# Optimization experiments

Measured on AMD Instinct MI355X. Metric: run time of the kernel, lower is better.

The kernel has to match this reference:

```python
import jax, jax.numpy as jnp
import numpy as np

N_NODES = 100000


def _gcn_conv(x, W, b, src, dst, deg_inv_sqrt):
    # linear transform first (PyG GCNConv order): [N, F] @ [F, H]
    h = x @ W
    # symmetric normalization per edge: deg^-1/2[src] * deg^-1/2[dst]
    norm = deg_inv_sqrt[src] * deg_inv_sqrt[dst]
    msg = h[src] * norm[:, None]  # [E, H]
    out = jax.ops.segment_sum(msg, dst, num_segments=N_NODES)
    return out + b


def setup_inputs() -> dict:
    key = jax.random.key(0)
    k1, k2, k3, k4 = jax.random.split(key, 4)
    F_IN, H = 512, 512
    E = 800000
    x = jax.random.normal(k1, (N_NODES, F_IN), dtype=jnp.float32)
    edge_index = jax.random.randint(k2, (2, E), 0, N_NODES, dtype=jnp.int64)
    W1 = jax.random.normal(k3, (F_IN, H), dtype=jnp.float32) * (1.0 / np.sqrt(F_IN))
    b1 = jnp.zeros((H,), dtype=jnp.float32)
    W2 = jax.random.normal(k4, (H, H), dtype=jnp.float32) * (1.0 / np.sqrt(H))
    b2 = jnp.zeros((H,), dtype=jnp.float32)
    return {"x": x, "edge_index": edge_index, "W1": W1, "b1": b1, "W2": W2, "b2": b2}


def reference(x, edge_index, W1, b1, W2, b2):
    # add self loops (PyG GCNConv default add_self_loops=True)
    loop = jnp.arange(N_NODES, dtype=edge_index.dtype)
    src = jnp.concatenate([edge_index[0], loop])
    dst = jnp.concatenate([edge_index[1], loop])
    # degree of destination nodes (including self loops)
    deg = jax.ops.segment_sum(jnp.ones_like(dst, dtype=x.dtype), dst, num_segments=N_NODES)
    deg_inv_sqrt = jnp.where(deg > 0, jax.lax.rsqrt(jnp.maximum(deg, 1.0)), 0.0)
    h = jax.nn.relu(_gcn_conv(x, W1, b1, src, dst, deg_inv_sqrt))
    # dropout is identity at inference (training=False)
    out = _gcn_conv(h, W2, b2, src, dst, deg_inv_sqrt)
    return out
```

## Files before the change

### kernel.cpp

```cpp
#include <hip/hip_runtime.h>

#define N_NODES 100000
#define E_EDGES 800000
#define E_TOT   900000
#define F 512

typedef __attribute__((ext_vector_type(8))) short short8;
typedef __attribute__((ext_vector_type(4))) float f32x4;
typedef unsigned int u32;

__device__ __forceinline__ float bfu(unsigned int u) {
    union { unsigned int i; float f; } c; c.i = u << 16; return c.f;
}
__device__ __forceinline__ unsigned short f2b(float f) {
    union { float f; unsigned int u; } c; c.f = f;
    return (unsigned short)((c.u + 0x7fffu + ((c.u >> 16) & 1u)) >> 16);
}
__device__ __forceinline__ float fbits(unsigned int u) {
    union { unsigned int i; float f; } c; c.i = u; return c.f;
}
__device__ __forceinline__ unsigned int bits(float f) {
    union { float f; unsigned int i; } c; c.f = f; return c.i;
}
__device__ __forceinline__ void gload_lds16(const void* g, void* l) {
    __builtin_amdgcn_global_load_lds(
        (const __attribute__((address_space(1))) u32*)g,
        (__attribute__((address_space(3))) u32*)l, 16, 0, 0);
}

__global__ void k_init(unsigned int* deg, unsigned int* counter) {
    int i = blockIdx.x * 256 + threadIdx.x;
    if (i < N_NODES) deg[i] = 1u;
    if (i == 0) *counter = 0u;
}

__global__ void k_hist(const int* __restrict__ ei, unsigned int* deg) {
    int e = blockIdx.x * 256 + threadIdx.x;
    if (e < E_EDGES) atomicAdd(&deg[ei[E_EDGES + e]], 1u);
}

__global__ void k_disalloc(const unsigned int* __restrict__ deg, unsigned int* counter,
                           float* __restrict__ dis,
                           int2* __restrict__ seg, unsigned int* __restrict__ cursor) {
    int i = blockIdx.x * 256 + threadIdx.x;
    if (i < N_NODES) {
        unsigned int d = deg[i];
        dis[i] = rsqrtf((float)d);
        unsigned int p = atomicAdd(counter, d);
        seg[i] = make_int2((int)p, (int)(p + d));
        cursor[i] = p;
    }
}

__global__ void k_scatter(const int* __restrict__ ei, const float* __restrict__ dis,
                          unsigned int* __restrict__ cursor,
                          uint2* __restrict__ ev) {
    int e = blockIdx.x * 256 + threadIdx.x;
    if (e < E_TOT) {
        int s, d;
        if (e < E_EDGES) { s = ei[e]; d = ei[E_EDGES + e]; }
        else             { s = e - E_EDGES; d = s; }
        unsigned int p = atomicAdd(&cursor[d], 1u);
        ev[p] = make_uint2((unsigned)s, bits(dis[s] * dis[d]));
    }
}

__global__ void k_cvtX(const float* __restrict__ xin, unsigned short* __restrict__ xb) {
    int i = blockIdx.x * 256 + threadIdx.x;
    const f32x4* p = (const f32x4*)xin + (size_t)i * 2;
    f32x4 a = __builtin_nontemporal_load(p);
    f32x4 b = __builtin_nontemporal_load(p + 1);
    uint4 o;
    o.x = (unsigned)f2b(a[0]) | ((unsigned)f2b(a[1]) << 16);
    o.y = (unsigned)f2b(a[2]) | ((unsigned)f2b(a[3]) << 16);
    o.z = (unsigned)f2b(b[0]) | ((unsigned)f2b(b[1]) << 16);
    o.w = (unsigned)f2b(b[2]) | ((unsigned)f2b(b[3]) << 16);
    *(uint4*)(xb + (size_t)i * 8) = o;
}

__global__ void k_cvtW(const float* __restrict__ W1, const float* __restrict__ W2,
                       unsigned short* __restrict__ W1t, unsigned short* __restrict__ W2t) {
    int t = blockIdx.x * 256 + threadIdx.x;
    int which = t >= F * F;
    int u = t - which * F * F;
    int n = u >> 9, k = u & 511;
    const float* W = which ? W2 : W1;
    unsigned short* Wt = which ? W2t : W1t;
    Wt[u] = f2b(W[k * F + n]);
}


#define STAGE_CHUNK(BUF, I, K0) { \
    gload_lds16(A + (size_t)ar[I] * F + (K0) + kcs[I], sm + (BUF) * 16384 + ((I) * 512 + t) * 8); \
    gload_lds16(Bt + (size_t)br[I] * F + (K0) + kcs[I], sm + 32768 + (BUF) * 16384 + ((I) * 512 + t) * 8); }

#define PHASE(BUF, I, WLIT, DOWAIT, DOSTAGE, K0N) { \
    if (DOSTAGE) { \
        STAGE_CHUNK((BUF) ^ 1, 2 * (I), K0N) \
        STAGE_CHUNK((BUF) ^ 1, 2 * (I) + 1, K0N) \
    } \
    if (DOWAIT) { asm volatile("s_waitcnt vmcnt(" #WLIT ")" ::: "memory"); } \
    __builtin_amdgcn_s_barrier(); \
    asm volatile("" ::: "memory"); \
    { \
        const unsigned short* la = sm + (BUF) * 16384; \
        const unsigned short* lb = sm + 32768 + (BUF) * 16384; \
        const int ksq = (I) >> 1, mhq = (I) & 1; \
        int koff = (ksq * 32 + khalf) ^ kx; \
        short8 af_[4]; \
        _Pragma("unroll") \
        for (int m4 = 0; m4 < 4; ++m4) \
            af_[m4] = *(const short8*)&la[(wr * 128 + (mhq * 4 + m4) * 16 + rsel) * 64 + koff]; \
        if (mhq == 0) { \
            _Pragma("unroll") \
            for (int n = 0; n < 4; ++n) \
                bfr[n] = *(const short8*)&lb[(wc * 64 + n * 16 + rsel) * 64 + koff]; \
        } \
        __builtin_amdgcn_s_setprio(1); \
        _Pragma("unroll") \
        for (int m4 = 0; m4 < 4; ++m4) \
            _Pragma("unroll") \
            for (int n = 0; n < 4; ++n) \
                acc[mhq * 4 + m4][n] = __builtin_amdgcn_mfma_f32_16x16x32_bf16(af_[m4], bfr[n], acc[mhq * 4 + m4][n], 0, 0, 0); \
        __builtin_amdgcn_s_setprio(0); \
    } \
    __builtin_amdgcn_s_barrier(); }

#define KTILE(BUF, K0N) \
    PHASE(BUF, 0, 4, 1, 1, K0N) PHASE(BUF, 1, 8, 0, 1, K0N) \
    PHASE(BUF, 2, 8, 0, 0, 0)   PHASE(BUF, 3, 8, 0, 0, 0)

__global__ __launch_bounds__(512, 2)
void gemm_bt(const unsigned short* __restrict__ A, const unsigned short* __restrict__ Bt,
             const float* __restrict__ bias,
             unsigned short* __restrict__ outb, float* __restrict__ outf,
             int relu, int M) {
    __shared__ unsigned short sm[65536];

    int nwg = gridDim.x * gridDim.y;
    int orig = blockIdx.y * gridDim.x + blockIdx.x;
    int q = nwg >> 3, r = nwg & 7;
    int xcd = orig & 7, j8 = orig >> 3;
    int wgid = (xcd < r ? xcd * (q + 1) : r * (q + 1) + (xcd - r) * q) + j8;
    int by = wgid & 1;
    int bx = wgid >> 1;

    int t  = threadIdx.x;
    int lane = t & 63, w = t >> 6;
    int wr = w >> 2, wc = w & 3;
    int rsel = lane & 15, khalf = (lane >> 4) * 8;
    int kx = (lane & 4) ? 16 : 0;

    f32x4 acc[8][4];
    #pragma unroll
    for (int m = 0; m < 8; ++m)
        #pragma unroll
        for (int n = 0; n < 4; ++n)
            acc[m][n] = (f32x4){0.f, 0.f, 0.f, 0.f};

    int rowBase = bx * 256;

    int ar[4], br[4], kcs[4];
    #pragma unroll
    for (int i = 0; i < 4; ++i) {
        int idx = i * 512 + t;
        int rr = idx >> 3;
        int kc = (idx & 7) * 8;
        kcs[i] = kc ^ ((rr & 4) ? 16 : 0);
        int ga = rowBase + rr; if (ga >= M) ga = M - 1;
        ar[i] = ga;
        br[i] = by * 256 + rr;
    }

    short8 bfr[4];

    STAGE_CHUNK(0, 0, 0) STAGE_CHUNK(0, 1, 0) STAGE_CHUNK(0, 2, 0) STAGE_CHUNK(0, 3, 0)

    KTILE(0,  64) KTILE(1, 128) KTILE(0, 192) KTILE(1, 256)
    KTILE(0, 320) KTILE(1, 384) KTILE(0, 448)
    PHASE(1, 0, 0, 1, 0, 0) PHASE(1, 1, 0, 0, 0, 0)
    PHASE(1, 2, 0, 0, 0, 0) PHASE(1, 3, 0, 0, 0, 0)

    int rq = (lane >> 4) * 4, cq = lane & 15;
    if (outb) {
        #pragma unroll
        for (int m = 0; m < 8; ++m)
            #pragma unroll
            for (int n = 0; n < 4; ++n) {
                int cl = wc * 64 + n * 16 + cq;
                float bv = bias[by * 256 + cl];
                #pragma unroll
                for (int j = 0; j < 4; ++j) {
                    int rl = wr * 128 + m * 16 + rq + j;
                    float v = acc[m][n][j] + bv;
                    if (relu) v = fmaxf(v, 0.f);
                    sm[rl * 256 + cl] = f2b(v);
                }
            }
        __syncthreads();
        #pragma unroll
        for (int p = 0; p < 16; ++p) {
            int sidx = p * 4096 + t * 8;
            int row = sidx >> 8;
            int col = sidx & 255;
            int grow = rowBase + row;
            if (grow < M) {
                uint4 v = *(const uint4*)&sm[sidx];
                *(uint4*)&outb[(size_t)grow * F + by * 256 + col] = v;
            }
        }
    } else {
        #pragma unroll
        for (int m = 0; m < 8; ++m)
            #pragma unroll
            for (int n = 0; n < 4; ++n) {
                int colv = by * 256 + wc * 64 + n * 16 + cq;
                float bv = bias[colv];
                #pragma unroll
                for (int j = 0; j < 4; ++j) {
                    int row = rowBase + wr * 128 + m * 16 + rq + j;
                    if (row < M) {
                        float v = acc[m][n][j] + bv;
                        if (relu) v = fmaxf(v, 0.f);
                        __builtin_nontemporal_store(v, outf + (size_t)row * F + colv);
                    }
                }
            }
    }
}

#define LOADP(k) uint2 p##k = ev[e + k]
#define LOADV(k) uint4 v##k = *(const uint4*)(base + ((size_t)p##k.x << 9))
#define ACCV(k)  { float w_ = fbits(p##k.y); \
    acc[0] += w_ * bfu(v##k.x & 0xffffu); acc[1] += w_ * bfu(v##k.x >> 16); \
    acc[2] += w_ * bfu(v##k.y & 0xffffu); acc[3] += w_ * bfu(v##k.y >> 16); \
    acc[4] += w_ * bfu(v##k.z & 0xffffu); acc[5] += w_ * bfu(v##k.z >> 16); \
    acc[6] += w_ * bfu(v##k.w & 0xffffu); acc[7] += w_ * bfu(v##k.w >> 16); }

__global__ __launch_bounds__(256)
void k_agg(const unsigned short* __restrict__ hin, const int2* __restrict__ seg,
           const uint2* __restrict__ ev,
           unsigned short* __restrict__ outb) {
    int node = blockIdx.x * 4 + (threadIdx.x >> 6);
    int lane = threadIdx.x & 63;
    if (node >= N_NODES) return;
    int2 se = seg[node];
    int e0 = se.x, e1 = se.y;
    float acc[8] = {0, 0, 0, 0, 0, 0, 0, 0};
    const unsigned short* base = hin + lane * 8;

    int e = e0;
    int n8 = e0 + ((e1 - e0) & ~7);
    for (; e < n8; e += 8) {
        LOADP(0); LOADP(1); LOADP(2); LOADP(3);
        LOADP(4); LOADP(5); LOADP(6); LOADP(7);
        LOADV(0); LOADV(1); LOADV(2); LOADV(3);
        LOADV(4); LOADV(5); LOADV(6); LOADV(7);
        ACCV(0); ACCV(1); ACCV(2); ACCV(3);
        ACCV(4); ACCV(5); ACCV(6); ACCV(7);
    }
    for (; e < e1; ++e) {
        LOADP(0); LOADV(0); ACCV(0);
    }

    uint4 o;
    o.x = (unsigned)f2b(acc[0]) | ((unsigned)f2b(acc[1]) << 16);
    o.y = (unsigned)f2b(acc[2]) | ((unsigned)f2b(acc[3]) << 16);
    o.z = (unsigned)f2b(acc[4]) | ((unsigned)f2b(acc[5]) << 16);
    o.w = (unsigned)f2b(acc[6]) | ((unsigned)f2b(acc[7]) << 16);
    *(uint4*)(outb + (size_t)node * F + lane * 8) = o;
}

extern "C" void kernel_launch(void* const* d_in, const int* in_sizes, int n_in,
                              void* d_out, int out_size, void* d_ws, size_t ws_size,
                              hipStream_t stream) {
    const float* x  = (const float*)d_in[0];
    const int*   ei = (const int*)d_in[1];
    const float* W1 = (const float*)d_in[2];
    const float* b1 = (const float*)d_in[3];
    const float* W2 = (const float*)d_in[4];
    const float* b2 = (const float*)d_in[5];
    float* out = (float*)d_out;

    char* ws = (char*)d_ws;
    size_t off = 0;
    auto alloc = [&](size_t bytes) -> void* {
        off = (off + 255) & ~(size_t)255;
        void* p = ws + off;
        off += bytes;
        return p;
    };

    unsigned short* tb  = (unsigned short*)alloc((size_t)N_NODES * F * 2);
    unsigned short* W1t = (unsigned short*)alloc((size_t)F * F * 2);
    unsigned short* W2t = (unsigned short*)alloc((size_t)F * F * 2);
    unsigned int*   deg = (unsigned int*)alloc((size_t)N_NODES * 4);
    float*          dis = (float*)alloc((size_t)N_NODES * 4);
    int2*           seg = (int2*)alloc((size_t)N_NODES * 8);
    unsigned int*   cur = (unsigned int*)alloc((size_t)N_NODES * 4);
    unsigned int*   cnt = (unsigned int*)alloc(256);
    uint2*          ev  = (uint2*)alloc((size_t)E_TOT * 8);

    unsigned short* h1b = (unsigned short*)d_out;
    unsigned short* xb  = (unsigned short*)((char*)d_out + (size_t)N_NODES * F * 2);

    int nb = (N_NODES + 255) / 256;

    k_init<<<nb, 256, 0, stream>>>(deg, cnt);
    k_hist<<<(E_EDGES + 255) / 256, 256, 0, stream>>>(ei, deg);
    k_disalloc<<<nb, 256, 0, stream>>>(deg, cnt, dis, seg, cur);
    k_scatter<<<(E_TOT + 255) / 256, 256, 0, stream>>>(ei, dis, cur, ev);

    k_cvtW<<<(2 * F * F) / 256, 256, 0, stream>>>(W1, W2, W1t, W2t);
    k_cvtX<<<(N_NODES * F / 8) / 256, 256, 0, stream>>>(x, xb);

    dim3 ggrid(2, (N_NODES + 255) / 256);

    k_agg<<<(N_NODES + 3) / 4, 256, 0, stream>>>(xb, seg, ev, tb);
    gemm_bt<<<ggrid, 512, 0, stream>>>(tb, W1t, b1, h1b, nullptr, 1, N_NODES);

    k_agg<<<(N_NODES + 3) / 4, 256, 0, stream>>>(h1b, seg, ev, tb);
    gemm_bt<<<ggrid, 512, 0, stream>>>(tb, W2t, b2, nullptr, out, 0, N_NODES);
}
```

Measured before the change: 645.7 us.

## Shrink GEMM tile to 256x128 with K=32 double-buffering for higher occupancy

```diff
diff --git a/kernel.cpp b/kernel.cpp
--- a/kernel.cpp
+++ b/kernel.cpp
@@ -89,136 +89,124 @@
     Wt[u] = f2b(W[k * F + n]);
 }
 
-
-#define STAGE_CHUNK(BUF, I, K0) { \
-    gload_lds16(A + (size_t)ar[I] * F + (K0) + kcs[I], sm + (BUF) * 16384 + ((I) * 512 + t) * 8); \
-    gload_lds16(Bt + (size_t)br[I] * F + (K0) + kcs[I], sm + 32768 + (BUF) * 16384 + ((I) * 512 + t) * 8); }
-
-#define PHASE(BUF, I, WLIT, DOWAIT, DOSTAGE, K0N) { \
-    if (DOSTAGE) { \
-        STAGE_CHUNK((BUF) ^ 1, 2 * (I), K0N) \
-        STAGE_CHUNK((BUF) ^ 1, 2 * (I) + 1, K0N) \
-    } \
-    if (DOWAIT) { asm volatile("s_waitcnt vmcnt(" #WLIT ")" ::: "memory"); } \
-    __builtin_amdgcn_s_barrier(); \
-    asm volatile("" ::: "memory"); \
-    { \
-        const unsigned short* la = sm + (BUF) * 16384; \
-        const unsigned short* lb = sm + 32768 + (BUF) * 16384; \
-        const int ksq = (I) >> 1, mhq = (I) & 1; \
-        int koff = (ksq * 32 + khalf) ^ kx; \
-        short8 af_[4]; \
-        _Pragma("unroll") \
-        for (int m4 = 0; m4 < 4; ++m4) \
-            af_[m4] = *(const short8*)&la[(wr * 128 + (mhq * 4 + m4) * 16 + rsel) * 64 + koff]; \
-        if (mhq == 0) { \
-            _Pragma("unroll") \
-            for (int n = 0; n < 4; ++n) \
-                bfr[n] = *(const short8*)&lb[(wc * 64 + n * 16 + rsel) * 64 + koff]; \
-        } \
-        __builtin_amdgcn_s_setprio(1); \
-        _Pragma("unroll") \
-        for (int m4 = 0; m4 < 4; ++m4) \
-            _Pragma("unroll") \
-            for (int n = 0; n < 4; ++n) \
-                acc[mhq * 4 + m4][n] = __builtin_amdgcn_mfma_f32_16x16x32_bf16(af_[m4], bfr[n], acc[mhq * 4 + m4][n], 0, 0, 0); \
-        __builtin_amdgcn_s_setprio(0); \
-    } \
-    __builtin_amdgcn_s_barrier(); }
-
-#define KTILE(BUF, K0N) \
-    PHASE(BUF, 0, 4, 1, 1, K0N) PHASE(BUF, 1, 8, 0, 1, K0N) \
-    PHASE(BUF, 2, 8, 0, 0, 0)   PHASE(BUF, 3, 8, 0, 0, 0)
-
-__global__ __launch_bounds__(512, 2)
+__global__ __launch_bounds__(512, 4)
 void gemm_bt(const unsigned short* __restrict__ A, const unsigned short* __restrict__ Bt,
              const float* __restrict__ bias,
              unsigned short* __restrict__ outb, float* __restrict__ outf,
              int relu, int M) {
-    __shared__ unsigned short sm[65536];
+    __shared__ unsigned short sm[24576];
 
     int nwg = gridDim.x * gridDim.y;
     int orig = blockIdx.y * gridDim.x + blockIdx.x;
     int q = nwg >> 3, r = nwg & 7;
     int xcd = orig & 7, j8 = orig >> 3;
     int wgid = (xcd < r ? xcd * (q + 1) : r * (q + 1) + (xcd - r) * q) + j8;
-    int by = wgid & 1;
-    int bx = wgid >> 1;
+    int by = wgid & 3;
+    int bx = wgid >> 2;
 
     int t  = threadIdx.x;
     int lane = t & 63, w = t >> 6;
-    int wr = w >> 2, wc = w & 3;
+    int wr = w >> 1, wc = w & 1;
     int rsel = lane & 15, khalf = (lane >> 4) * 8;
-    int kx = (lane & 4) ? 16 : 0;
-
-    f32x4 acc[8][4];
+
+    f32x4 acc[4][4];
     #pragma unroll
-    for (int m = 0; m < 8; ++m)
+    for (int m = 0; m < 4; ++m)
         #pragma unroll
         for (int n = 0; n < 4; ++n)
             acc[m][n] = (f32x4){0.f, 0.f, 0.f, 0.f};
 
     int rowBase = bx * 256;
 
-    int ar[4], br[4], kcs[4];
+    int arA[2], kcA[2];
     #pragma unroll
-    for (int i = 0; i < 4; ++i) {
+    for (int i = 0; i < 2; ++i) {
         int idx = i * 512 + t;
-        int rr = idx >> 3;
-        int kc = (idx & 7) * 8;
-        kcs[i] = kc ^ ((rr & 4) ? 16 : 0);
+        int rr = idx >> 2;
+        kcA[i] = (idx & 3) * 8;
         int ga = rowBase + rr; if (ga >= M) ga = M - 1;
-        ar[i] = ga;
-        br[i] = by * 256 + rr;
-    }
-
-    short8 bfr[4];
-
-    STAGE_CHUNK(0, 0, 0) STAGE_CHUNK(0, 1, 0) STAGE_CHUNK(0, 2, 0) STAGE_CHUNK(0, 3, 0)
-
-    KTILE(0,  64) KTILE(1, 128) KTILE(0, 192) KTILE(1, 256)
-    KTILE(0, 320) KTILE(1, 384) KTILE(0, 448)
-    PHASE(1, 0, 0, 1, 0, 0) PHASE(1, 1, 0, 0, 0, 0)
-    PHASE(1, 2, 0, 0, 0, 0) PHASE(1, 3, 0, 0, 0, 0)
+        arA[i] = ga;
+    }
+    int brB = by * 128 + (t >> 2);
+    int kcB = (t & 3) * 8;
+
+    auto STAGE = [&](int buf, int k0) {
+        gload_lds16(A + (size_t)arA[0] * F + k0 + kcA[0], sm + buf * 8192 + t * 8);
+        gload_lds16(A + (size_t)arA[1] * F + k0 + kcA[1], sm + buf * 8192 + (512 + t) * 8);
+        gload_lds16(Bt + (size_t)brB * F + k0 + kcB, sm + 16384 + buf * 4096 + t * 8);
+    };
+    auto COMPUTE = [&](int buf) {
+        const unsigned short* la = sm + buf * 8192;
+        const unsigned short* lb = sm + 16384 + buf * 4096;
+        short8 bfr[4];
+        #pragma unroll
+        for (int n = 0; n < 4; ++n)
+            bfr[n] = *(const short8*)&lb[(wc * 64 + n * 16 + rsel) * 32 + khalf];
+        #pragma unroll
+        for (int m = 0; m < 4; ++m) {
+            short8 af = *(const short8*)&la[(wr * 64 + m * 16 + rsel) * 32 + khalf];
+            #pragma unroll
+            for (int n = 0; n < 4; ++n)
+                acc[m][n] = __builtin_amdgcn_mfma_f32_16x16x32_bf16(af, bfr[n], acc[m][n], 0, 0, 0);
+        }
+    };
+
+    STAGE(0, 0);
+    __syncthreads();
+    #pragma unroll
+    for (int kp = 0; kp < 8; ++kp) {
+        STAGE(1, (2 * kp + 1) * 32);
+        COMPUTE(0);
+        __syncthreads();
+        if (kp < 7) STAGE(0, (2 * kp + 2) * 32);
+        COMPUTE(1);
+        __syncthreads();
+    }
 
     int rq = (lane >> 4) * 4, cq = lane & 15;
     if (outb) {
         #pragma unroll
-        for (int m = 0; m < 8; ++m)
+        for (int h = 0; h < 2; ++h) {
+            if (h) __syncthreads();
+            if ((wr >> 1) == h) {
+                #pragma unroll
+                for (int m = 0; m < 4; ++m)
+                    #pragma unroll
+                    for (int n = 0; n < 4; ++n) {
+                        int cl = wc * 64 + n * 16 + cq;
+                        float bv = bias[by * 128 + cl];
+                        #pragma unroll
+                        for (int j = 0; j < 4; ++j) {
+                            int rl = (wr & 1) * 64 + m * 16 + rq + j;
+                            float v = acc[m][n][j] + bv;
+                            if (relu) v = fmaxf(v, 0.f);
+                            sm[rl * 128 + cl] = f2b(v);
+                        }
+                    }
+            }
+            __syncthreads();
             #pragma unroll
-            for (int n = 0; n < 4; ++n) {
-                int cl = wc * 64 + n * 16 + cq;
-                float bv = bias[by * 256 + cl];
-                #pragma unroll
-                for (int j = 0; j < 4; ++j) {
-                    int rl = wr * 128 + m * 16 + rq + j;
-                    float v = acc[m][n][j] + bv;
-                    if (relu) v = fmaxf(v, 0.f);
-                    sm[rl * 256 + cl] = f2b(v);
+            for (int p = 0; p < 4; ++p) {
+                int sidx = (p * 512 + t) * 8;
+                int row = sidx >> 7;
+                int col = sidx & 127;
+                int grow = rowBase + h * 128 + row;
+                if (grow < M) {
+                    uint4 v = *(const uint4*)&sm[sidx];
+                    *(uint4*)&outb[(size_t)grow * F + by * 128 + col] = v;
                 }
-            }
-        __syncthreads();
-        #pragma unroll
-        for (int p = 0; p < 16; ++p) {
-            int sidx = p * 4096 + t * 8;
-            int row = sidx >> 8;
-            int col = sidx & 255;
-            int grow = rowBase + row;
-            if (grow < M) {
-                uint4 v = *(const uint4*)&sm[sidx];
-                *(uint4*)&outb[(size_t)grow * F + by * 256 + col] = v;
             }
         }
     } else {
         #pragma unroll
-        for (int m = 0; m < 8; ++m)
+        for (int m = 0; m < 4; ++m)
             #pragma unroll
             for (int n = 0; n < 4; ++n) {
-                int colv = by * 256 + wc * 64 + n * 16 + cq;
+                int colv = by * 128 + wc * 64 + n * 16 + cq;
                 float bv = bias[colv];
                 #pragma unroll
                 for (int j = 0; j < 4; ++j) {
-                    int row = rowBase + wr * 128 + m * 16 + rq + j;
+                    int row = rowBase + wr * 64 + m * 16 + rq + j;
                     if (row < M) {
                         float v = acc[m][n][j] + bv;
                         if (relu) v = fmaxf(v, 0.f);
@@ -314,7 +302,7 @@
     k_cvtW<<<(2 * F * F) / 256, 256, 0, stream>>>(W1, W2, W1t, W2t);
     k_cvtX<<<(N_NODES * F / 8) / 256, 256, 0, stream>>>(x, xb);
 
-    dim3 ggrid(2, (N_NODES + 255) / 256);
+    dim3 ggrid(4, (N_NODES + 255) / 256);
 
     k_agg<<<(N_NODES + 3) / 4, 256, 0, stream>>>(xb, seg, ev, tb);
     gemm_bt<<<ggrid, 512, 0, stream>>>(tb, W1t, b1, h1b, nullptr, 1, N_NODES);
```

After: 617.9 us. 4.3% less time.
